# Performance work log

Measured on AMD Instinct MI355X. Metric: run time of the kernel, lower is better.

Reference implementation:

```python
import jax, jax.numpy as jnp
import numpy as np

D_MODEL = 768
N_HEADS = 12
D_HEAD = D_MODEL // N_HEADS
B, L = 2, 4096


def setup_inputs() -> dict:
    key = jax.random.key(0)
    k1, k2, k3 = jax.random.split(key, 3)
    scale = 1.0 / np.sqrt(D_MODEL)
    return {
        "x": jax.random.normal(k1, (B, L, D_MODEL), dtype=jnp.float32),
        "w_qkv": jax.random.normal(k2, (D_MODEL, 3 * D_MODEL), dtype=jnp.float32) * scale,
        "b_qkv": jnp.zeros((3 * D_MODEL,), dtype=jnp.float32),
        "w_out": jax.random.normal(k3, (D_MODEL, D_MODEL), dtype=jnp.float32) * scale,
        "b_out": jnp.zeros((D_MODEL,), dtype=jnp.float32),
    }


def reference(x, w_qkv, b_qkv, w_out, b_out):
    b, l, d = x.shape
    # qkv projection -> (B, L, 3, H, Dh) -> split
    qkv = (x @ w_qkv + b_qkv).reshape(b, l, 3, N_HEADS, D_HEAD)
    qkv = jnp.transpose(qkv, (2, 0, 3, 1, 4))  # (3, B, H, L, Dh)
    q, k, v = qkv[0], qkv[1], qkv[2]
    # scaled scores with causal mask (dropout=0 / eval mode)
    att = jnp.einsum("bhqd,bhkd->bhqk", q, k) * (D_HEAD ** -0.5)
    causal = jnp.tril(jnp.ones((l, l), dtype=bool))
    att = jnp.where(causal, att, -jnp.inf)
    att = jax.nn.softmax(att, axis=-1)
    out = jnp.einsum("bhqk,bhkd->bhqd", att, v)  # (B, H, L, Dh)
    out = jnp.transpose(out, (0, 2, 1, 3)).reshape(b, l, d)
    return out @ w_out + b_out
```

## Files before the change

kernel.cpp:

```cpp
#include <hip/hip_runtime.h>
#include <hip/hip_bf16.h>

#define D_MODEL 768
#define NH 12
#define DHd 64
#define NB 2
#define SL 4096
#define BLr (NB*SL)
#define N3 (3*D_MODEL)
#define QSCALE 0.18033688011112042f

typedef __bf16 bf16x8 __attribute__((ext_vector_type(8)));
typedef float f32x4 __attribute__((ext_vector_type(4)));
typedef float f32x16 __attribute__((ext_vector_type(16)));
typedef unsigned int u32x4 __attribute__((ext_vector_type(4)));

__device__ __forceinline__ unsigned short f2bf(float f) {
  unsigned int u = __float_as_uint(f);
  u = (u + 0x7FFFu + ((u >> 16) & 1u)) >> 16;
  return (unsigned short)u;
}
__device__ __forceinline__ unsigned short bfc(float f) {
  __bf16 h = (__bf16)f;
  return __builtin_bit_cast(unsigned short, h);
}
__device__ __forceinline__ float fexp2(float x) {
  float r; asm("v_exp_f32 %0, %1" : "=v"(r) : "v"(x)); return r;
}
__device__ __forceinline__ unsigned int pk2(float lo, float hi2) {
  unsigned int r;
  asm("v_cvt_pk_bf16_f32 %0, %1, %2" : "=v"(r) : "v"(lo), "v"(hi2));
  return r;
}
__device__ __forceinline__ void gload_lds16(const void* g, void* l) {
  __builtin_amdgcn_global_load_lds(
      (const __attribute__((address_space(1))) void*)g,
      (__attribute__((address_space(3))) void*)l, 16, 0, 0);
}

__global__ __launch_bounds__(256) void cast_f32_bf16(const float* __restrict__ in,
                                                     unsigned short* __restrict__ out, int n4) {
  int i = blockIdx.x * 256 + threadIdx.x;
  if (i >= n4) return;
  float4 v = reinterpret_cast<const float4*>(in)[i];
  ushort4 o;
  o.x = f2bf(v.x); o.y = f2bf(v.y); o.z = f2bf(v.z); o.w = f2bf(v.w);
  reinterpret_cast<ushort4*>(out)[i] = o;
}

__global__ __launch_bounds__(256) void transpose_cast2(const float* __restrict__ wq,
                                                       unsigned short* __restrict__ oq,
                                                       const float* __restrict__ wo,
                                                       unsigned short* __restrict__ oo) {
  __shared__ float t[32][33];
  const int bx = blockIdx.x;
  const float* in; unsigned short* out; int R, C, c0;
  if (bx < 72) { in = wq; out = oq; R = 768; C = 2304; c0 = bx * 32; }
  else         { in = wo; out = oo; R = 768; C = 768;  c0 = (bx - 72) * 32; }
  int r0 = blockIdx.y * 32;
  int tx = threadIdx.x & 31, ty = threadIdx.x >> 5;
  #pragma unroll
  for (int i = 0; i < 32; i += 8) t[ty + i][tx] = in[(size_t)(r0 + ty + i) * C + c0 + tx];
  __syncthreads();
  #pragma unroll
  for (int i = 0; i < 32; i += 8) out[(size_t)(c0 + ty + i) * R + r0 + tx] = f2bf(t[tx][ty + i]);
}

__global__ __launch_bounds__(256) void gemm_qkv(const unsigned short* __restrict__ A,
                                                const unsigned short* __restrict__ Bt,
                                                const float* __restrict__ bias,
                                                unsigned short* __restrict__ Qf,
                                                unsigned short* __restrict__ Kf,
                                                unsigned short* __restrict__ Vf,
                                                int M, int N, int Kdim) {
  __shared__ unsigned short As[128 * 32];
  __shared__ unsigned short Bs[128 * 32];
  const int tid = threadIdx.x;
  const int lane = tid & 63, wave = tid >> 6;
  const int tm = blockIdx.x * 128, tn = blockIdx.y * 128;
  const int wm = (wave >> 1) * 64, wn = (wave & 1) * 64;
  const int fr = lane & 15, fk8 = (lane >> 4) * 8;
  const int srow = wave * 32 + (lane >> 2);
  const int scol = (lane & 3) * 8;

  f32x4 acc[4][4] = {};

  for (int k0 = 0; k0 < Kdim; k0 += 32) {
    __syncthreads();
    gload_lds16(A  + (size_t)(tm + srow)      * Kdim + k0 + scol, As + (wave * 32)      * 32);
    gload_lds16(A  + (size_t)(tm + srow + 16) * Kdim + k0 + scol, As + (wave * 32 + 16) * 32);
    gload_lds16(Bt + (size_t)(tn + srow)      * Kdim + k0 + scol, Bs + (wave * 32)      * 32);
    gload_lds16(Bt + (size_t)(tn + srow + 16) * Kdim + k0 + scol, Bs + (wave * 32 + 16) * 32);
    __syncthreads();

    bf16x8 af[4], bfr[4];
    #pragma unroll
    for (int i = 0; i < 4; i++) {
      af[i]  = *(const bf16x8*)(As + (wm + i * 16 + fr) * 32 + fk8);
      bfr[i] = *(const bf16x8*)(Bs + (wn + i * 16 + fr) * 32 + fk8);
    }
    #pragma unroll
    for (int i = 0; i < 4; i++)
      #pragma unroll
      for (int j = 0; j < 4; j++)
        acc[i][j] = __builtin_amdgcn_mfma_f32_16x16x32_bf16(af[i], bfr[j], acc[i][j], 0, 0, 0);
  }

  const int fq = (lane >> 4) * 4;
  #pragma unroll
  for (int j = 0; j < 4; j++) {
    int col = tn + wn + j * 16 + fr;
    float bv = bias[col];
    int which = col / D_MODEL;
    int hd = col % D_MODEL;
    int h = hd >> 6, d = hd & 63;
    #pragma unroll
    for (int i = 0; i < 4; i++) {
      #pragma unroll
      for (int r = 0; r < 4; r++) {
        int row = tm + wm + i * 16 + fq + r;
        int b = row >> 12, l = row & 4095;
        float v = acc[i][j][r] + bv;
        size_t hb = (size_t)b * NH + h;
        if (which == 2) {
          size_t off = ((hb * 64 + (l >> 6)) * 8 + ((l >> 4) & 3) * 2 + (d >> 5)) * 512
                     + (size_t)((d & 31) + 32 * ((l >> 2) & 1)) * 8
                     + ((l & 3) + 4 * ((l >> 3) & 1));
          Vf[off] = bfc(v);
        } else {
          size_t off = ((hb * 128 + (l >> 5)) * 4 + (d >> 4)) * 512
                     + (size_t)((l & 31) + 32 * ((d >> 3) & 1)) * 8 + (d & 7);
          if (which == 0) Qf[off] = bfc(v * QSCALE);
          else            Kf[off] = bfc(v);
        }
      }
    }
  }
}

__global__ __launch_bounds__(128) void gemm_out(const unsigned short* __restrict__ A,
                                                const unsigned short* __restrict__ Bt,
                                                const float* __restrict__ bias,
                                                float* __restrict__ Out,
                                                int M, int N, int Kdim) {
  __shared__ unsigned short As[128 * 32];
  __shared__ unsigned short Bs[64 * 32];
  const int tid = threadIdx.x;
  const int lane = tid & 63, wave = tid >> 6;
  const int tm = blockIdx.x * 128, tn = blockIdx.y * 64;
  const int wm = wave * 64;
  const int fr = lane & 15, fk8 = (lane >> 4) * 8;
  const int srA = wave * 64 + (lane >> 2);
  const int srB = wave * 32 + (lane >> 2);
  const int scol = (lane & 3) * 8;

  f32x4 acc[4][4] = {};

  for (int k0 = 0; k0 < Kdim; k0 += 32) {
    __syncthreads();
    gload_lds16(A  + (size_t)(tm + srA)      * Kdim + k0 + scol, As + (wave * 64)      * 32);
    gload_lds16(A  + (size_t)(tm + srA + 16) * Kdim + k0 + scol, As + (wave * 64 + 16) * 32);
    gload_lds16(A  + (size_t)(tm + srA + 32) * Kdim + k0 + scol, As + (wave * 64 + 32) * 32);
    gload_lds16(A  + (size_t)(tm + srA + 48) * Kdim + k0 + scol, As + (wave * 64 + 48) * 32);
    gload_lds16(Bt + (size_t)(tn + srB)      * Kdim + k0 + scol, Bs + (wave * 32)      * 32);
    gload_lds16(Bt + (size_t)(tn + srB + 16) * Kdim + k0 + scol, Bs + (wave * 32 + 16) * 32);
    __syncthreads();

    bf16x8 af[4], bfr[4];
    #pragma unroll
    for (int i = 0; i < 4; i++) {
      af[i]  = *(const bf16x8*)(As + (wm + i * 16 + fr) * 32 + fk8);
      bfr[i] = *(const bf16x8*)(Bs + (i * 16 + fr) * 32 + fk8);
    }
    #pragma unroll
    for (int i = 0; i < 4; i++)
      #pragma unroll
      for (int j = 0; j < 4; j++)
        acc[i][j] = __builtin_amdgcn_mfma_f32_16x16x32_bf16(af[i], bfr[j], acc[i][j], 0, 0, 0);
  }

  const int fq = (lane >> 4) * 4;
  #pragma unroll
  for (int i = 0; i < 4; i++)
    #pragma unroll
    for (int j = 0; j < 4; j++) {
      int col = tn + j * 16 + fr;
      float bv = bias[col];
      #pragma unroll
      for (int r = 0; r < 4; r++) {
        int row = tm + wm + i * 16 + fq + r;
        Out[(size_t)row * N + col] = acc[i][j][r] + bv;
      }
    }
}

#define PVSTEP(P, B, VB0, VB1) do {                                        \
    u32x4 w4;                                                              \
    w4[0] = pk2(P[(B)+0], P[(B)+1]);                                       \
    w4[1] = pk2(P[(B)+2], P[(B)+3]);                                       \
    w4[2] = pk2(P[(B)+4], P[(B)+5]);                                       \
    w4[3] = pk2(P[(B)+6], P[(B)+7]);                                       \
    bf16x8 pa = __builtin_bit_cast(bf16x8, w4);                            \
    oacc0 = __builtin_amdgcn_mfma_f32_32x32x16_bf16(pa, VB0, oacc0, 0,0,0);\
    oacc1 = __builtin_amdgcn_mfma_f32_32x32x16_bf16(pa, VB1, oacc1, 0,0,0);\
    lacc  = __builtin_amdgcn_mfma_f32_32x32x16_bf16(pa, onesB, lacc, 0,0,0);\
  } while(0)

__global__ __launch_bounds__(128) void attn_fwd(const unsigned short* __restrict__ Qf,
                                                const unsigned short* __restrict__ Kf,
                                                const unsigned short* __restrict__ Vf,
                                                unsigned short* __restrict__ O) {
  const int bid = blockIdx.x;
  const int t = 63 - (bid / 48);
  const int r48 = bid % 48;
  const int bh = r48 % 24;
  const int s = r48 / 24;
  const int tid = threadIdx.x;
  const int w = tid >> 6;
  const int lane = tid & 63;
  const int l31 = lane & 31, hi = lane >> 5;
  const int Cm1 = 2 * t + s;

  __shared__ float LoA[16][64];
  __shared__ float LoB[16][64];
  __shared__ float Lsum[2][32];

  const char* Kbh = (const char*)Kf + ((size_t)bh * 512) * 1024 + lane * 16;
  const char* Vbh = (const char*)Vf + ((size_t)bh * 512) * 1024 + lane * 16;
  const int b = bh / NH, h = bh % NH;

  bf16x8 qf[4];
  const char* Qb_ = (const char*)Qf + (((size_t)bh * 128 + t * 2 + s) * 4) * 1024 + lane * 16;
  #pragma unroll
  for (int f = 0; f < 4; f++) qf[f] = *(const bf16x8*)(Qb_ + f * 1024);

  unsigned int ow = (l31 == 0) ? 0x3F803F80u : 0u;
  u32x4 o4; o4[0] = ow; o4[1] = ow; o4[2] = ow; o4[3] = ow;
  const bf16x8 onesB = __builtin_bit_cast(bf16x8, o4);

  f32x16 zf = {};
  f32x16 oacc0 = {}, oacc1 = {}, lacc = {};

  for (int c = w; c <= Cm1; c += 2) {
    const char* kp = Kbh + (size_t)c * 4096;
    bf16x8 kf0 = *(const bf16x8*)(kp);
    bf16x8 kf1 = *(const bf16x8*)(kp + 1024);
    bf16x8 kf2 = *(const bf16x8*)(kp + 2048);
    bf16x8 kf3 = *(const bf16x8*)(kp + 3072);
    const char* vp = Vbh + (size_t)c * 4096;
    bf16x8 v0a = *(const bf16x8*)(vp);
    bf16x8 v0b = *(const bf16x8*)(vp + 1024);

    __builtin_amdgcn_s_setprio(1);
    f32x16 sS = __builtin_amdgcn_mfma_f32_32x32x16_bf16(kf0, qf[0], zf, 0, 0, 0);
    sS = __builtin_amdgcn_mfma_f32_32x32x16_bf16(kf1, qf[1], sS, 0, 0, 0);
    sS = __builtin_amdgcn_mfma_f32_32x32x16_bf16(kf2, qf[2], sS, 0, 0, 0);
    sS = __builtin_amdgcn_mfma_f32_32x32x16_bf16(kf3, qf[3], sS, 0, 0, 0);
    __builtin_amdgcn_s_setprio(0);

    if (c == Cm1) {
      #pragma unroll
      for (int r = 0; r < 16; r++) {
        int kvo = (r & 3) + 8 * (r >> 2) + 4 * hi;
        if (kvo > l31) sS[r] = -1e30f;
      }
    }

    #pragma unroll
    for (int r = 0; r < 16; r++) sS[r] = fexp2(sS[r]);

    __builtin_amdgcn_s_setprio(1);
    PVSTEP(sS, 0, v0a, v0b);
    {
      bf16x8 v1a = *(const bf16x8*)(vp + 2048);
      bf16x8 v1b = *(const bf16x8*)(vp + 3072);
      PVSTEP(sS, 8, v1a, v1b);
    }
    __builtin_amdgcn_s_setprio(0);
  }

  if (l31 == 0) {
    #pragma unroll
    for (int r = 0; r < 16; r++)
      Lsum[w][(r & 3) + 8 * (r >> 2) + 4 * hi] = lacc[r];
  }
  if (w == 1) {
    #pragma unroll
    for (int r = 0; r < 16; r++) {
      LoA[r][lane] = oacc0[r];
      LoB[r][lane] = oacc1[r];
    }
  }
  __syncthreads();

  if (w == 0) {
    float lm = Lsum[0][l31] + Lsum[1][l31];
    const int q0w = t * 64 + s * 32;
    #pragma unroll
    for (int r = 0; r < 16; r++) {
      int qo = (r & 3) + 8 * (r >> 2) + 4 * hi;
      float linv = 1.0f / __shfl(lm, qo);
      float o0 = (oacc0[r] + LoA[r][lane]) * linv;
      float o1 = (oacc1[r] + LoB[r][lane]) * linv;
      size_t base = ((size_t)b * SL + q0w + qo) * D_MODEL + h * DHd;
      O[base + l31]      = bfc(o0);
      O[base + 32 + l31] = bfc(o1);
    }
  }
}

extern "C" void kernel_launch(void* const* d_in, const int* in_sizes, int n_in,
                              void* d_out, int out_size, void* d_ws, size_t ws_size,
                              hipStream_t stream) {
  (void)in_sizes; (void)n_in; (void)out_size; (void)ws_size;
  const float* x     = (const float*)d_in[0];
  const float* w_qkv = (const float*)d_in[1];
  const float* b_qkv = (const float*)d_in[2];
  const float* w_out = (const float*)d_in[3];
  const float* b_out = (const float*)d_in[4];
  float* out = (float*)d_out;

  unsigned short* p = (unsigned short*)d_ws;
  unsigned short* xb    = p; p += (size_t)BLr * D_MODEL;
  unsigned short* wqkvT = p; p += (size_t)N3 * D_MODEL;
  unsigned short* woutT = p; p += (size_t)D_MODEL * D_MODEL;
  unsigned short* Qf    = p; p += (size_t)NB * NH * SL * DHd;
  unsigned short* Kf    = p; p += (size_t)NB * NH * SL * DHd;
  unsigned short* Vf    = p; p += (size_t)NB * NH * SL * DHd;
  unsigned short* Ob    = p;

  cast_f32_bf16<<<(BLr * D_MODEL / 4 + 255) / 256, 256, 0, stream>>>(x, xb, BLr * D_MODEL / 4);
  transpose_cast2<<<dim3(96, 24), 256, 0, stream>>>(w_qkv, wqkvT, w_out, woutT);
  gemm_qkv<<<dim3(BLr / 128, N3 / 128), 256, 0, stream>>>(xb, wqkvT, b_qkv, Qf, Kf, Vf,
                                                          BLr, N3, D_MODEL);
  attn_fwd<<<3072, 128, 0, stream>>>(Qf, Kf, Vf, Ob);
  gemm_out<<<dim3(BLr / 128, D_MODEL / 64), 128, 0, stream>>>(Ob, woutT, b_out, out,
                                                              BLr, D_MODEL, D_MODEL);
}
```

Measured before the change: 175.7 us.

## Share K/V tiles across query halves via double-buffered LDS staging

Result: slower. 219.4 us (+24.9%).

```diff
diff --git a/kernel.cpp b/kernel.cpp
--- a/kernel.cpp
+++ b/kernel.cpp
@@ -211,22 +211,20 @@
                                                 const unsigned short* __restrict__ Vf,
                                                 unsigned short* __restrict__ O) {
   const int bid = blockIdx.x;
-  const int t = 63 - (bid / 48);
-  const int r48 = bid % 48;
-  const int bh = r48 % 24;
-  const int s = r48 / 24;
+  const int t = 63 - (bid / 24);
+  const int bh = bid % 24;
   const int tid = threadIdx.x;
-  const int w = tid >> 6;
+  const int s = tid >> 6;
   const int lane = tid & 63;
   const int l31 = lane & 31, hi = lane >> 5;
-  const int Cm1 = 2 * t + s;
-
-  __shared__ float LoA[16][64];
-  __shared__ float LoB[16][64];
+  const int Cmax = 2 * t + 1;
+  const int myC = 2 * t + s;
+
+  __shared__ unsigned short KVs[2][4096];
   __shared__ float Lsum[2][32];
 
-  const char* Kbh = (const char*)Kf + ((size_t)bh * 512) * 1024 + lane * 16;
-  const char* Vbh = (const char*)Vf + ((size_t)bh * 512) * 1024 + lane * 16;
+  const char* Kbh = (const char*)Kf + ((size_t)bh * 512) * 1024;
+  const char* Vbh = (const char*)Vf + ((size_t)bh * 512) * 1024;
   const int b = bh / NH, h = bh % NH;
 
   bf16x8 qf[4];
@@ -241,15 +239,26 @@
   f32x16 zf = {};
   f32x16 oacc0 = {}, oacc1 = {}, lacc = {};
 
-  for (int c = w; c <= Cm1; c += 2) {
-    const char* kp = Kbh + (size_t)c * 4096;
-    bf16x8 kf0 = *(const bf16x8*)(kp);
-    bf16x8 kf1 = *(const bf16x8*)(kp + 1024);
-    bf16x8 kf2 = *(const bf16x8*)(kp + 2048);
-    bf16x8 kf3 = *(const bf16x8*)(kp + 3072);
-    const char* vp = Vbh + (size_t)c * 4096;
-    bf16x8 v0a = *(const bf16x8*)(vp);
-    bf16x8 v0b = *(const bf16x8*)(vp + 1024);
+  auto stage = [&](int buf, int c) {
+    const char* kg = Kbh + (size_t)c * 4096 + s * 2048 + lane * 16;
+    const char* vg = Vbh + (size_t)c * 4096 + s * 2048 + lane * 16;
+    char* lk = (char*)&KVs[buf][0]    + s * 2048;
+    char* lv = (char*)&KVs[buf][2048] + s * 2048;
+    gload_lds16(kg,        lk);
+    gload_lds16(kg + 1024, lk + 1024);
+    gload_lds16(vg,        lv);
+    gload_lds16(vg + 1024, lv + 1024);
+  };
+
+  auto body = [&](int buf, int c) {
+    const char* lk = (const char*)&KVs[buf][0]    + lane * 16;
+    const char* lv = (const char*)&KVs[buf][2048] + lane * 16;
+    bf16x8 kf0 = *(const bf16x8*)(lk);
+    bf16x8 kf1 = *(const bf16x8*)(lk + 1024);
+    bf16x8 kf2 = *(const bf16x8*)(lk + 2048);
+    bf16x8 kf3 = *(const bf16x8*)(lk + 3072);
+    bf16x8 v0a = *(const bf16x8*)(lv);
+    bf16x8 v0b = *(const bf16x8*)(lv + 1024);
 
     __builtin_amdgcn_s_setprio(1);
     f32x16 sS = __builtin_amdgcn_mfma_f32_32x32x16_bf16(kf0, qf[0], zf, 0, 0, 0);
@@ -258,7 +267,7 @@
     sS = __builtin_amdgcn_mfma_f32_32x32x16_bf16(kf3, qf[3], sS, 0, 0, 0);
     __builtin_amdgcn_s_setprio(0);
 
-    if (c == Cm1) {
+    if (c == myC) {
       #pragma unroll
       for (int r = 0; r < 16; r++) {
         int kvo = (r & 3) + 8 * (r >> 2) + 4 * hi;
@@ -272,40 +281,38 @@
     __builtin_amdgcn_s_setprio(1);
     PVSTEP(sS, 0, v0a, v0b);
     {
-      bf16x8 v1a = *(const bf16x8*)(vp + 2048);
-      bf16x8 v1b = *(const bf16x8*)(vp + 3072);
+      bf16x8 v1a = *(const bf16x8*)(lv + 2048);
+      bf16x8 v1b = *(const bf16x8*)(lv + 3072);
       PVSTEP(sS, 8, v1a, v1b);
     }
     __builtin_amdgcn_s_setprio(0);
+  };
+
+  stage(0, 0);
+  __syncthreads();
+  for (int c = 0; c <= Cmax; ++c) {
+    int cur = c & 1;
+    if (c < Cmax) stage(cur ^ 1, c + 1);
+    if (c <= myC) body(cur, c);
+    __syncthreads();
   }
 
   if (l31 == 0) {
     #pragma unroll
     for (int r = 0; r < 16; r++)
-      Lsum[w][(r & 3) + 8 * (r >> 2) + 4 * hi] = lacc[r];
-  }
-  if (w == 1) {
-    #pragma unroll
-    for (int r = 0; r < 16; r++) {
-      LoA[r][lane] = oacc0[r];
-      LoB[r][lane] = oacc1[r];
-    }
+      Lsum[s][(r & 3) + 8 * (r >> 2) + 4 * hi] = lacc[r];
   }
   __syncthreads();
 
-  if (w == 0) {
-    float lm = Lsum[0][l31] + Lsum[1][l31];
-    const int q0w = t * 64 + s * 32;
-    #pragma unroll
-    for (int r = 0; r < 16; r++) {
-      int qo = (r & 3) + 8 * (r >> 2) + 4 * hi;
-      float linv = 1.0f / __shfl(lm, qo);
-      float o0 = (oacc0[r] + LoA[r][lane]) * linv;
-      float o1 = (oacc1[r] + LoB[r][lane]) * linv;
-      size_t base = ((size_t)b * SL + q0w + qo) * D_MODEL + h * DHd;
-      O[base + l31]      = bfc(o0);
-      O[base + 32 + l31] = bfc(o1);
-    }
+  float lm = Lsum[s][l31];
+  const int q0w = t * 64 + s * 32;
+  #pragma unroll
+  for (int r = 0; r < 16; r++) {
+    int qo = (r & 3) + 8 * (r >> 2) + 4 * hi;
+    float linv = 1.0f / __shfl(lm, qo);
+    size_t base = ((size_t)b * SL + q0w + qo) * D_MODEL + h * DHd;
+    O[base + l31]      = bfc(oacc0[r] * linv);
+    O[base + 32 + l31] = bfc(oacc1[r] * linv);
   }
 }
 
@@ -333,7 +340,7 @@
   transpose_cast2<<<dim3(96, 24), 256, 0, stream>>>(w_qkv, wqkvT, w_out, woutT);
   gemm_qkv<<<dim3(BLr / 128, N3 / 128), 256, 0, stream>>>(xb, wqkvT, b_qkv, Qf, Kf, Vf,
                                                           BLr, N3, D_MODEL);
-  attn_fwd<<<3072, 128, 0, stream>>>(Qf, Kf, Vf, Ob);
+  attn_fwd<<<1536, 128, 0, stream>>>(Qf, Kf, Vf, Ob);
   gemm_out<<<dim3(BLr / 128, D_MODEL / 64), 128, 0, stream>>>(Ob, woutT, b_out, out,
                                                               BLr, D_MODEL, D_MODEL);
 }
```

## Stage Q/K epilogue through LDS for vector stores and prefetch next K tile

Applied to the files above, without the earlier changes.

After: 190.9 us. 8.6% more time.

```diff
diff --git a/kernel.cpp b/kernel.cpp
--- a/kernel.cpp
+++ b/kernel.cpp
@@ -73,8 +73,9 @@
                                                 unsigned short* __restrict__ Kf,
                                                 unsigned short* __restrict__ Vf,
                                                 int M, int N, int Kdim) {
-  __shared__ unsigned short As[128 * 32];
-  __shared__ unsigned short Bs[128 * 32];
+  __shared__ unsigned short smem[128 * 136];
+  unsigned short* As = smem;
+  unsigned short* Bs = smem + 128 * 32;
   const int tid = threadIdx.x;
   const int lane = tid & 63, wave = tid >> 6;
   const int tm = blockIdx.x * 128, tn = blockIdx.y * 128;
@@ -107,31 +108,58 @@
   }
 
   const int fq = (lane >> 4) * 4;
-  #pragma unroll
-  for (int j = 0; j < 4; j++) {
-    int col = tn + wn + j * 16 + fr;
-    float bv = bias[col];
-    int which = col / D_MODEL;
-    int hd = col % D_MODEL;
-    int h = hd >> 6, d = hd & 63;
-    #pragma unroll
-    for (int i = 0; i < 4; i++) {
-      #pragma unroll
-      for (int r = 0; r < 4; r++) {
-        int row = tm + wm + i * 16 + fq + r;
-        int b = row >> 12, l = row & 4095;
-        float v = acc[i][j][r] + bv;
-        size_t hb = (size_t)b * NH + h;
-        if (which == 2) {
+  const int which = tn / D_MODEL;
+  if (which != 2) {
+    const float qs = (which == 0) ? QSCALE : 1.0f;
+    unsigned short* Dst = (which == 0) ? Qf : Kf;
+    __syncthreads();
+    #pragma unroll
+    for (int j = 0; j < 4; j++) {
+      int lc = wn + j * 16 + fr;
+      float bv = bias[tn + lc];
+      #pragma unroll
+      for (int i = 0; i < 4; i++)
+        #pragma unroll
+        for (int r = 0; r < 4; r++)
+          smem[(wm + i * 16 + fq + r) * 136 + lc] = bfc((acc[i][j][r] + bv) * qs);
+    }
+    __syncthreads();
+    const int T = tid >> 3;
+    const int T_l = T >> 3, T_d = T & 7;
+    const int h_off = T_d >> 2, d4 = T_d & 3;
+    const int b0 = tm >> 12;
+    const int l0 = (tm & 4095) + T_l * 32;
+    const int h0 = (tn % D_MODEL) >> 6;
+    const size_t hb = (size_t)b0 * NH + h0 + h_off;
+    unsigned short* tbase = Dst + ((hb * 128 + (l0 >> 5)) * 4 + d4) * 512;
+    const int u = tid & 7;
+    #pragma unroll
+    for (int c = 0; c < 8; c++) {
+      int idx8 = u * 8 + c;
+      int l5 = idx8 & 31, dd = idx8 >> 5;
+      int lc = h_off * 64 + d4 * 16 + dd * 8;
+      ulonglong2 v16 = *(const ulonglong2*)(smem + (T_l * 32 + l5) * 136 + lc);
+      *(ulonglong2*)(tbase + idx8 * 8) = v16;
+    }
+  } else {
+    #pragma unroll
+    for (int j = 0; j < 4; j++) {
+      int col = tn + wn + j * 16 + fr;
+      float bv = bias[col];
+      int hd = col % D_MODEL;
+      int h = hd >> 6, d = hd & 63;
+      #pragma unroll
+      for (int i = 0; i < 4; i++) {
+        #pragma unroll
+        for (int r = 0; r < 4; r++) {
+          int row = tm + wm + i * 16 + fq + r;
+          int b = row >> 12, l = row & 4095;
+          float v = acc[i][j][r] + bv;
+          size_t hb = (size_t)b * NH + h;
           size_t off = ((hb * 64 + (l >> 6)) * 8 + ((l >> 4) & 3) * 2 + (d >> 5)) * 512
                      + (size_t)((d & 31) + 32 * ((l >> 2) & 1)) * 8
                      + ((l & 3) + 4 * ((l >> 3) & 1));
           Vf[off] = bfc(v);
-        } else {
-          size_t off = ((hb * 128 + (l >> 5)) * 4 + (d >> 4)) * 512
-                     + (size_t)((l & 31) + 32 * ((d >> 3) & 1)) * 8 + (d & 7);
-          if (which == 0) Qf[off] = bfc(v * QSCALE);
-          else            Kf[off] = bfc(v);
         }
       }
     }
@@ -194,6 +222,8 @@
     }
 }
 
+struct K4 { bf16x8 k[4]; };
+
 #define PVSTEP(P, B, VB0, VB1) do {                                        \
     u32x4 w4;                                                              \
     w4[0] = pk2(P[(B)+0], P[(B)+1]);                                       \
@@ -238,24 +268,28 @@
   u32x4 o4; o4[0] = ow; o4[1] = ow; o4[2] = ow; o4[3] = ow;
   const bf16x8 onesB = __builtin_bit_cast(bf16x8, o4);
 
-  f32x16 zf = {};
   f32x16 oacc0 = {}, oacc1 = {}, lacc = {};
 
-  for (int c = w; c <= Cm1; c += 2) {
+  auto loadK = [&](K4& kk, int c) {
     const char* kp = Kbh + (size_t)c * 4096;
-    bf16x8 kf0 = *(const bf16x8*)(kp);
-    bf16x8 kf1 = *(const bf16x8*)(kp + 1024);
-    bf16x8 kf2 = *(const bf16x8*)(kp + 2048);
-    bf16x8 kf3 = *(const bf16x8*)(kp + 3072);
+    kk.k[0] = *(const bf16x8*)(kp);
+    kk.k[1] = *(const bf16x8*)(kp + 1024);
+    kk.k[2] = *(const bf16x8*)(kp + 2048);
+    kk.k[3] = *(const bf16x8*)(kp + 3072);
+  };
+
+  auto body = [&](const K4& cur, K4* nxt, int c) {
     const char* vp = Vbh + (size_t)c * 4096;
     bf16x8 v0a = *(const bf16x8*)(vp);
     bf16x8 v0b = *(const bf16x8*)(vp + 1024);
-
+    if (nxt) loadK(*nxt, c + 2);
+
+    f32x16 sS = {};
     __builtin_amdgcn_s_setprio(1);
-    f32x16 sS = __builtin_amdgcn_mfma_f32_32x32x16_bf16(kf0, qf[0], zf, 0, 0, 0);
-    sS = __builtin_amdgcn_mfma_f32_32x32x16_bf16(kf1, qf[1], sS, 0, 0, 0);
-    sS = __builtin_amdgcn_mfma_f32_32x32x16_bf16(kf2, qf[2], sS, 0, 0, 0);
-    sS = __builtin_amdgcn_mfma_f32_32x32x16_bf16(kf3, qf[3], sS, 0, 0, 0);
+    sS = __builtin_amdgcn_mfma_f32_32x32x16_bf16(cur.k[0], qf[0], sS, 0, 0, 0);
+    sS = __builtin_amdgcn_mfma_f32_32x32x16_bf16(cur.k[1], qf[1], sS, 0, 0, 0);
+    sS = __builtin_amdgcn_mfma_f32_32x32x16_bf16(cur.k[2], qf[2], sS, 0, 0, 0);
+    sS = __builtin_amdgcn_mfma_f32_32x32x16_bf16(cur.k[3], qf[3], sS, 0, 0, 0);
     __builtin_amdgcn_s_setprio(0);
 
     if (c == Cm1) {
@@ -277,6 +311,19 @@
       PVSTEP(sS, 8, v1a, v1b);
     }
     __builtin_amdgcn_s_setprio(0);
+  };
+
+  if (w <= Cm1) {
+    K4 kA, kB;
+    loadK(kA, w);
+    int c = w; bool useA = true;
+    for (;;) {
+      bool hasNext = (c + 2 <= Cm1);
+      if (useA) body(kA, hasNext ? &kB : nullptr, c);
+      else      body(kB, hasNext ? &kA : nullptr, c);
+      if (!hasNext) break;
+      c += 2; useA = !useA;
+    }
   }
 
   if (l31 == 0) {
```
